# Kernel optimization log

Hardware: AMD Instinct MI355X
Metric: run time of the kernel (lower is better)

Reference implementation:

```python
import jax, jax.numpy as jnp
import numpy as np

N = 50000          # nodes
E = 1600000        # edges (avg degree 32)
F_IN = 128         # input feature dim
H = 8              # attention heads
D = 8              # per-head dim (concat -> H*D = 64)
NEG_SLOPE = 0.2    # PyG GATConv leaky relu slope


def setup_inputs() -> dict:
    key = jax.random.key(0)
    ks = jax.random.split(key, 16)
    x = jax.random.normal(ks[0], (N, F_IN), jnp.float32)
    edge_index = jax.random.randint(ks[1], (2, E), 0, N, jnp.int32)
    inp = {"x": x, "edge_index": edge_index}
    fin = F_IN
    for i in range(4):
        inp[f"W{i}"] = jax.random.normal(ks[2 + 3 * i], (fin, H * D), jnp.float32) * (1.0 / np.sqrt(fin))
        inp[f"att{i}"] = jax.random.normal(ks[3 + 3 * i], (2, H, D), jnp.float32) * 0.1
        inp[f"b{i}"] = jnp.zeros((H * D,), jnp.float32)
        fin = H * D
    return inp


def gat_layer(x, W, att, b, src, dst):
    # linear projection -> per-head features [N, H, D]
    h = (x @ W).reshape(-1, H, D)
    # per-node attention logits for src/dst roles [N, H]
    e_src = jnp.einsum("nhd,hd->nh", h, att[0])
    e_dst = jnp.einsum("nhd,hd->nh", h, att[1])
    # per-edge score [E, H]
    e = jax.nn.leaky_relu(e_src[src] + e_dst[dst], NEG_SLOPE)
    # segment softmax over incoming edges of each dst node
    m = jax.ops.segment_max(e, dst, num_segments=N)
    w = jnp.exp(e - m[dst])
    s = jax.ops.segment_sum(w, dst, num_segments=N)
    alpha = w / (s[dst] + 1e-16)
    # weighted message scatter-add: [E,H,D] -> [N,H,D]
    msg = alpha[:, :, None] * h[src]
    out = jax.ops.segment_sum(msg, dst, num_segments=N)
    return out.reshape(-1, H * D) + b


def reference(x, edge_index, W0, att0, b0, W1, att1, b1, W2, att2, b2, W3, att3, b3):
    src, dst = edge_index[0], edge_index[1]
    h = x
    params = [(W0, att0, b0), (W1, att1, b1), (W2, att2, b2), (W3, att3, b3)]
    for i, (W, att, b) in enumerate(params):
        h = gat_layer(h, W, att, b, src, dst)
        if i < len(params) - 1:
            h = jax.nn.elu(h)  # inter-layer activation as in PyG GAT (default ELU)
    return h
```

## Files before the change

### kernel.cpp

```cpp
#include <hip/hip_runtime.h>

#define N_NODES 50000
#define N_EDGES 1600000
#define HD 64
#define NH 8
#define NBKT 196
#define EPB 8192
#define GB1 196
#define SCAN_M (NBKT * GB1)
#define NB2 151
#define DCAP 8960
#define SEGB 2048
#define GBN 196

__device__ inline int wave_incl_scan(int v, int lane) {
#pragma unroll
    for (int o = 1; o < 64; o <<= 1) {
        int t = __shfl_up(v, o);
        if (lane >= o) v += t;
    }
    return v;
}

template <int F>
__device__ __forceinline__ void gemm_body16(
    int bx, int by, int t,
    const float* __restrict__ x, const float* __restrict__ W,
    const float* __restrict__ att,
    _Float16* __restrict__ h, float* __restrict__ es, float* __restrict__ ed) {
    int n = bx * 256 + t;
    int f0 = by * 16;
    int nc = (n < N_NODES) ? n : (N_NODES - 1);
    const float4* xrow = (const float4*)x + (size_t)nc * (F / 4);
    float acc[16];
#pragma unroll
    for (int i = 0; i < 16; i++) acc[i] = 0.f;
#pragma unroll 4
    for (int kk = 0; kk < F / 4; kk++) {
        float4 xv = xrow[kk];
        const float* Wk = W + (kk * 4) * 64 + f0;
#pragma unroll
        for (int i = 0; i < 16; i++)
            acc[i] += xv.x * Wk[i] + xv.y * Wk[64 + i] +
                      xv.z * Wk[128 + i] + xv.w * Wk[192 + i];
    }
    if (n >= N_NODES) return;

    float s0 = 0.f, s1 = 0.f, d0 = 0.f, d1 = 0.f;
#pragma unroll
    for (int i = 0; i < 8; i++) {
        s0 += acc[i] * att[f0 + i];
        d0 += acc[i] * att[64 + f0 + i];
    }
#pragma unroll
    for (int i = 8; i < 16; i++) {
        s1 += acc[i] * att[f0 + i];
        d1 += acc[i] * att[64 + f0 + i];
    }
    int hh = f0 >> 3;
    es[n * NH + hh] = s0; es[n * NH + hh + 1] = s1;
    ed[n * NH + hh] = d0; ed[n * NH + hh + 1] = d1;

    union { _Float16 hf[16]; uint4 u[2]; } cv;
#pragma unroll
    for (int i = 0; i < 16; i++) cv.hf[i] = (_Float16)acc[i];
    uint4* hp = (uint4*)(h + (size_t)n * HD + f0);
    hp[0] = cv.u[0];
    hp[1] = cv.u[1];
}

template <int F>
__global__ __launch_bounds__(256) void gemm_att_kernel(
    const float* __restrict__ x, const float* __restrict__ W,
    const float* __restrict__ att,
    _Float16* __restrict__ h, float* __restrict__ es, float* __restrict__ ed) {
    gemm_body16<F>(blockIdx.x, blockIdx.y, threadIdx.x, x, W, att, h, es, ed);
}

__global__ __launch_bounds__(256) void histA_gemm_kernel(
    const int* __restrict__ dst, int* __restrict__ offs,
    const float* __restrict__ x, const float* __restrict__ W,
    const float* __restrict__ att,
    _Float16* __restrict__ h, float* __restrict__ es, float* __restrict__ ed) {
    if (blockIdx.y < 4) {
        gemm_body16<128>(blockIdx.x, blockIdx.y, threadIdx.x, x, W, att, h, es, ed);
        return;
    }
    int bb = blockIdx.x;
    __shared__ int hist[NBKT];
    int t = threadIdx.x;
    if (t < NBKT) hist[t] = 0;
    __syncthreads();
    int base = bb * EPB;
#pragma unroll
    for (int k = 0; k < EPB / 256; k++) {
        int e = base + k * 256 + t;
        if (e < N_EDGES) atomicAdd(&hist[dst[e] >> 8], 1);
    }
    __syncthreads();
    if (t < NBKT) offs[t * GB1 + bb] = hist[t];
}

__global__ __launch_bounds__(256) void scanB1_kernel(int* __restrict__ offs,
                                                     int* __restrict__ part2) {
    __shared__ int wsum[4];
    int t = threadIdx.x, lane = t & 63, wv = t >> 6;
    int i = blockIdx.x * 256 + t;
    int v = (i < SCAN_M) ? offs[i] : 0;
    int inc = wave_incl_scan(v, lane);
    if (lane == 63) wsum[wv] = inc;
    __syncthreads();
    if (t == 0) {
        int a = 0;
        for (int k = 0; k < 4; k++) { int x = wsum[k]; wsum[k] = a; a += x; }
    }
    __syncthreads();
    int excl = wsum[wv] + inc - v;
    if (i < SCAN_M) offs[i] = excl;
    if (t == 255) part2[blockIdx.x] = wsum[wv] + inc;
}

__global__ __launch_bounds__(256) void scatC_kernel(const int* __restrict__ src,
                                                    const int* __restrict__ dst,
                                                    const int* __restrict__ offs,
                                                    const int* __restrict__ part2,
                                                    unsigned* __restrict__ ebuf) {
    __shared__ int cur[NBKT];
    __shared__ int base_s[NBKT];
    __shared__ int p2s[256];
    __shared__ int p2w[4];
    int t = threadIdx.x, lane = t & 63, wv = t >> 6;
    int v = (t < NB2) ? part2[t] : 0;
    int inc = wave_incl_scan(v, lane);
    if (lane == 63) p2w[wv] = inc;
    __syncthreads();
    if (t == 0) {
        int a = 0;
        for (int k = 0; k < 4; k++) { int x = p2w[k]; p2w[k] = a; a += x; }
    }
    __syncthreads();
    p2s[t] = p2w[wv] + inc - v;
    if (t < NBKT) cur[t] = 0;
    __syncthreads();
    if (t < NBKT) {
        int f = t * GB1 + blockIdx.x;
        base_s[t] = offs[f] + p2s[f >> 8];
    }
    __syncthreads();
    int base = blockIdx.x * EPB;
#pragma unroll
    for (int k = 0; k < EPB / 256; k++) {
        int e = base + k * 256 + t;
        if (e < N_EDGES) {
            int d = dst[e];
            int b = d >> 8;
            int r = atomicAdd(&cur[b], 1);
            ebuf[base_s[b] + r] = (unsigned)src[e] | ((unsigned)(d & 255) << 16);
        }
    }
}

__global__ __launch_bounds__(512) void csrD_kernel(const int* __restrict__ offs,
                                                   const int* __restrict__ part2,
                                                   const unsigned* __restrict__ ebuf,
                                                   int* __restrict__ rowptr,
                                                   unsigned short* __restrict__ csr) {
    __shared__ unsigned eb[DCAP];
    __shared__ int hist[SEGB];
    __shared__ int wsum[8];
    __shared__ int p2s[512];
    int b = blockIdx.x, t = threadIdx.x;
    int lane = t & 63, wv = t >> 6;
    {
        int v = (t < NB2) ? part2[t] : 0;
        int inc = wave_incl_scan(v, lane);
        if (lane == 63) wsum[wv] = inc;
        __syncthreads();
        if (t == 0) {
            int a = 0;
            for (int k = 0; k < 8; k++) { int x = wsum[k]; wsum[k] = a; a += x; }
        }
        __syncthreads();
        p2s[t] = wsum[wv] + inc - v;
        __syncthreads();
    }
    int f0 = b * GB1;
    int base = offs[f0] + p2s[f0 >> 8];
    int nxt;
    if (b == NBKT - 1) nxt = N_EDGES;
    else { int f1 = (b + 1) * GB1; nxt = offs[f1] + p2s[f1 >> 8]; }
    int nb = nxt - base;
    if (nb > DCAP) nb = DCAP;
    for (int i = t; i < SEGB; i += 512) hist[i] = 0;
    __syncthreads();
    for (int i = t; i < nb; i += 512) {
        unsigned v = ebuf[base + i];
        eb[i] = v;
        int bin = (int)((v >> 16) << 3) | (int)((v & 0xFFFFu) >> 13);
        atomicAdd(&hist[bin], 1);
    }
    __syncthreads();
    int b0 = t << 2;
    int loc0 = hist[b0], loc1 = hist[b0 + 1], loc2 = hist[b0 + 2], loc3 = hist[b0 + 3];
    int s = loc0 + loc1 + loc2 + loc3;
    int inc = wave_incl_scan(s, lane);
    if (lane == 63) wsum[wv] = inc;
    __syncthreads();
    if (t == 0) {
        int a = 0;
        for (int k = 0; k < 8; k++) { int x = wsum[k]; wsum[k] = a; a += x; }
    }
    __syncthreads();
    int run = wsum[wv] + inc - s;
    hist[b0] = run; run += loc0;
    hist[b0 + 1] = run; run += loc1;
    hist[b0 + 2] = run; run += loc2;
    hist[b0 + 3] = run;
    __syncthreads();
    if (t < 256) {
        int node = b * 256 + t;
        if (node < N_NODES) rowptr[node] = base + hist[t << 3];
    }
    if (b == 0 && t == 0) rowptr[N_NODES] = N_EDGES;
    __syncthreads();
    for (int i = t; i < nb; i += 512) {
        unsigned v = eb[i];
        int bin = (int)((v >> 16) << 3) | (int)((v & 0xFFFFu) >> 13);
        int r = atomicAdd(&hist[bin], 1);
        csr[base + r] = (unsigned short)(v & 0xFFFFu);
    }
}

__global__ __launch_bounds__(256) void agg_kernel(
    const uint4* __restrict__ h8, const float* __restrict__ es,
    const float* __restrict__ ed, const int* __restrict__ rowptr,
    const unsigned short* __restrict__ csr, const float4* __restrict__ b4,
    float4* __restrict__ out4, int apply_elu) {
    int t = threadIdx.x;
    int wv = t >> 6, L = t & 63;
    int n = blockIdx.x * 8 + wv * 2 + (L >> 5);
    int g = (L >> 3) & 3, o = L & 7;
    int beg = rowptr[n], end = rowptr[n + 1];
    float edn = ed[n * NH + o];
    int last = (end > beg) ? (end - 1) : 0;
    float acc[8] = {0.f, 0.f, 0.f, 0.f, 0.f, 0.f, 0.f, 0.f};
    float ssum = 0.f;
    int j = beg;
    for (; j + 16 <= end; j += 16) {
        int s0 = csr[j + g];
        int s1 = csr[j + 4 + g];
        int s2 = csr[j + 8 + g];
        int s3 = csr[j + 12 + g];
        uint4 hv0 = h8[s0 * 8 + o];
        uint4 hv1 = h8[s1 * 8 + o];
        uint4 hv2 = h8[s2 * 8 + o];
        uint4 hv3 = h8[s3 * 8 + o];
        float ev0 = es[s0 * NH + o];
        float ev1 = es[s1 * NH + o];
        float ev2 = es[s2 * NH + o];
        float ev3 = es[s3 * NH + o];
        float e0 = ev0 + edn; e0 = (e0 > 0.f) ? e0 : 0.2f * e0;
        float e1 = ev1 + edn; e1 = (e1 > 0.f) ? e1 : 0.2f * e1;
        float e2 = ev2 + edn; e2 = (e2 > 0.f) ? e2 : 0.2f * e2;
        float e3 = ev3 + edn; e3 = (e3 > 0.f) ? e3 : 0.2f * e3;
        float w0 = __expf(e0), w1 = __expf(e1);
        float w2 = __expf(e2), w3 = __expf(e3);
        union { uint4 u; _Float16 f[8]; } c0, c1, c2, c3;
        c0.u = hv0; c1.u = hv1; c2.u = hv2; c3.u = hv3;
#pragma unroll
        for (int i = 0; i < 8; i++) {
            acc[i] += w0 * (float)c0.f[i] + w1 * (float)c1.f[i];
            acc[i] += w2 * (float)c2.f[i] + w3 * (float)c3.f[i];
        }
        ssum += w0 + w1;
        ssum += w2 + w3;
    }
    if (j < end) {
        int i0 = j + g, i1 = j + 4 + g, i2 = j + 8 + g, i3 = j + 12 + g;
        int s0 = csr[(i0 < end) ? i0 : last];
        int s1 = csr[(i1 < end) ? i1 : last];
        int s2 = csr[(i2 < end) ? i2 : last];
        int s3 = csr[(i3 < end) ? i3 : last];
        uint4 hv0 = h8[s0 * 8 + o];
        uint4 hv1 = h8[s1 * 8 + o];
        uint4 hv2 = h8[s2 * 8 + o];
        uint4 hv3 = h8[s3 * 8 + o];
        float ev0 = es[s0 * NH + o];
        float ev1 = es[s1 * NH + o];
        float ev2 = es[s2 * NH + o];
        float ev3 = es[s3 * NH + o];
        float e0 = ev0 + edn; e0 = (e0 > 0.f) ? e0 : 0.2f * e0;
        float e1 = ev1 + edn; e1 = (e1 > 0.f) ? e1 : 0.2f * e1;
        float e2 = ev2 + edn; e2 = (e2 > 0.f) ? e2 : 0.2f * e2;
        float e3 = ev3 + edn; e3 = (e3 > 0.f) ? e3 : 0.2f * e3;
        float w0 = (i0 < end) ? __expf(e0) : 0.f;
        float w1 = (i1 < end) ? __expf(e1) : 0.f;
        float w2 = (i2 < end) ? __expf(e2) : 0.f;
        float w3 = (i3 < end) ? __expf(e3) : 0.f;
        union { uint4 u; _Float16 f[8]; } c0, c1, c2, c3;
        c0.u = hv0; c1.u = hv1; c2.u = hv2; c3.u = hv3;
#pragma unroll
        for (int i = 0; i < 8; i++) {
            acc[i] += w0 * (float)c0.f[i] + w1 * (float)c1.f[i];
            acc[i] += w2 * (float)c2.f[i] + w3 * (float)c3.f[i];
        }
        ssum += w0 + w1;
        ssum += w2 + w3;
    }
#pragma unroll
    for (int i = 0; i < 8; i++) {
        acc[i] += __shfl_xor(acc[i], 8);
        acc[i] += __shfl_xor(acc[i], 16);
    }
    ssum += __shfl_xor(ssum, 8);
    ssum += __shfl_xor(ssum, 16);

    if (g == 0) {
        float inv = 1.f / (ssum + 1e-16f);
        float4 bv0 = b4[2 * o], bv1 = b4[2 * o + 1];
        float4 r0, r1;
        r0.x = acc[0] * inv + bv0.x; r0.y = acc[1] * inv + bv0.y;
        r0.z = acc[2] * inv + bv0.z; r0.w = acc[3] * inv + bv0.w;
        r1.x = acc[4] * inv + bv1.x; r1.y = acc[5] * inv + bv1.y;
        r1.z = acc[6] * inv + bv1.z; r1.w = acc[7] * inv + bv1.w;
        if (apply_elu) {
            r0.x = (r0.x > 0.f) ? r0.x : (__expf(r0.x) - 1.f);
            r0.y = (r0.y > 0.f) ? r0.y : (__expf(r0.y) - 1.f);
            r0.z = (r0.z > 0.f) ? r0.z : (__expf(r0.z) - 1.f);
            r0.w = (r0.w > 0.f) ? r0.w : (__expf(r0.w) - 1.f);
            r1.x = (r1.x > 0.f) ? r1.x : (__expf(r1.x) - 1.f);
            r1.y = (r1.y > 0.f) ? r1.y : (__expf(r1.y) - 1.f);
            r1.z = (r1.z > 0.f) ? r1.z : (__expf(r1.z) - 1.f);
            r1.w = (r1.w > 0.f) ? r1.w : (__expf(r1.w) - 1.f);
        }
        out4[n * 16 + 2 * o] = r0;
        out4[n * 16 + 2 * o + 1] = r1;
    }
}

extern "C" void kernel_launch(void* const* d_in, const int* in_sizes, int n_in,
                              void* d_out, int out_size, void* d_ws, size_t ws_size,
                              hipStream_t stream) {
    const float* x   = (const float*)d_in[0];
    const int*   ei  = (const int*)d_in[1];
    const int*   src = ei;
    const int*   dst = ei + N_EDGES;
    const float* W[4]   = {(const float*)d_in[2], (const float*)d_in[5],
                           (const float*)d_in[8], (const float*)d_in[11]};
    const float* att[4] = {(const float*)d_in[3], (const float*)d_in[6],
                           (const float*)d_in[9], (const float*)d_in[12]};
    const float* bb[4]  = {(const float*)d_in[4], (const float*)d_in[7],
                           (const float*)d_in[10], (const float*)d_in[13]};

    char* wsb = (char*)d_ws;
    size_t off = 0;
    auto alloc = [&](size_t bytes) -> void* {
        size_t a = (off + 255) & ~(size_t)255;
        off = a + bytes;
        return (void*)(wsb + a);
    };
    int*            offs   = (int*)alloc((size_t)SCAN_M * 4);
    int*            part2  = (int*)alloc((size_t)NB2 * 4);
    unsigned*       ebuf   = (unsigned*)alloc((size_t)N_EDGES * 4);
    int*            rowptr = (int*)alloc((size_t)(N_NODES + 1) * 4);
    unsigned short* csr    = (unsigned short*)alloc((size_t)N_EDGES * 2);
    _Float16*       h      = (_Float16*)alloc((size_t)N_NODES * HD * 2);
    float*          es     = (float*)alloc((size_t)N_NODES * NH * 4);
    float*          ed     = (float*)alloc((size_t)N_NODES * NH * 4);
    float*          act0   = (float*)alloc((size_t)N_NODES * HD * 4);
    float*          act1   = (float*)alloc((size_t)N_NODES * HD * 4);

    const int GA = N_NODES / 8;
    const dim3 GG(GBN, 4);
    const dim3 GF(GBN, 5);

    histA_gemm_kernel<<<GF, 256, 0, stream>>>(dst, offs, x, W[0], att[0],
                                              h, es, ed);
    scanB1_kernel<<<NB2, 256, 0, stream>>>(offs, part2);
    scatC_kernel<<<GB1, 256, 0, stream>>>(src, dst, offs, part2, ebuf);
    csrD_kernel<<<NBKT, 512, 0, stream>>>(offs, part2, ebuf, rowptr, csr);

    agg_kernel<<<GA, 256, 0, stream>>>((const uint4*)h, es, ed, rowptr, csr,
                                       (const float4*)bb[0], (float4*)act0, 1);
    gemm_att_kernel<64><<<GG, 256, 0, stream>>>(act0, W[1], att[1], h, es, ed);
    agg_kernel<<<GA, 256, 0, stream>>>((const uint4*)h, es, ed, rowptr, csr,
                                       (const float4*)bb[1], (float4*)act1, 1);
    gemm_att_kernel<64><<<GG, 256, 0, stream>>>(act1, W[2], att[2], h, es, ed);
    agg_kernel<<<GA, 256, 0, stream>>>((const uint4*)h, es, ed, rowptr, csr,
                                       (const float4*)bb[2], (float4*)act0, 1);
    gemm_att_kernel<64><<<GG, 256, 0, stream>>>(act0, W[3], att[3], h, es, ed);
    agg_kernel<<<GA, 256, 0, stream>>>((const uint4*)h, es, ed, rowptr, csr,
                                       (const float4*)bb[3], (float4*)d_out, 0);
}
```

Measured before the change: 335.1 us.

## Fuse aggregation with next layer's projection and attention logits

Merges each inter-layer aggregation kernel with the following 64x64 projection and attention-logit kernel. Each block loads the next layer's weights into shared memory, aggregates 8 nodes and applies ELU into shared memory, then computes the projected fp16 features and per-head es/ed directly. This removes three kernel launches and the fp32 activation write and re-read between layers. In exchange it double-buffers h/es/ed and adds a per-block weight load into roughly 17 KB of shared memory, which may lower occupancy for the latency-bound gather.

```diff
diff --git a/kernel.cpp b/kernel.cpp
--- a/kernel.cpp
+++ b/kernel.cpp
@@ -67,14 +67,6 @@
     uint4* hp = (uint4*)(h + (size_t)n * HD + f0);
     hp[0] = cv.u[0];
     hp[1] = cv.u[1];
-}
-
-template <int F>
-__global__ __launch_bounds__(256) void gemm_att_kernel(
-    const float* __restrict__ x, const float* __restrict__ W,
-    const float* __restrict__ att,
-    _Float16* __restrict__ h, float* __restrict__ es, float* __restrict__ ed) {
-    gemm_body16<F>(blockIdx.x, blockIdx.y, threadIdx.x, x, W, att, h, es, ed);
 }
 
 __global__ __launch_bounds__(256) void histA_gemm_kernel(
@@ -231,89 +223,92 @@
     }
 }
 
+#define AGG_LOOP()                                                          \
+    int beg = rowptr[n], end = rowptr[n + 1];                               \
+    float edn = ed_in[n * NH + o];                                          \
+    int last = (end > beg) ? (end - 1) : 0;                                 \
+    float acc[8] = {0.f, 0.f, 0.f, 0.f, 0.f, 0.f, 0.f, 0.f};                \
+    float ssum = 0.f;                                                       \
+    int j = beg;                                                            \
+    for (; j + 16 <= end; j += 16) {                                        \
+        int s0 = csr[j + g];                                                \
+        int s1 = csr[j + 4 + g];                                            \
+        int s2 = csr[j + 8 + g];                                            \
+        int s3 = csr[j + 12 + g];                                           \
+        uint4 hv0 = h8[s0 * 8 + o];                                         \
+        uint4 hv1 = h8[s1 * 8 + o];                                         \
+        uint4 hv2 = h8[s2 * 8 + o];                                         \
+        uint4 hv3 = h8[s3 * 8 + o];                                         \
+        float ev0 = es_in[s0 * NH + o];                                     \
+        float ev1 = es_in[s1 * NH + o];                                     \
+        float ev2 = es_in[s2 * NH + o];                                     \
+        float ev3 = es_in[s3 * NH + o];                                     \
+        float e0 = ev0 + edn; e0 = (e0 > 0.f) ? e0 : 0.2f * e0;             \
+        float e1 = ev1 + edn; e1 = (e1 > 0.f) ? e1 : 0.2f * e1;             \
+        float e2 = ev2 + edn; e2 = (e2 > 0.f) ? e2 : 0.2f * e2;             \
+        float e3 = ev3 + edn; e3 = (e3 > 0.f) ? e3 : 0.2f * e3;             \
+        float w0 = __expf(e0), w1 = __expf(e1);                             \
+        float w2 = __expf(e2), w3 = __expf(e3);                             \
+        union { uint4 u; _Float16 f[8]; } c0, c1, c2, c3;                   \
+        c0.u = hv0; c1.u = hv1; c2.u = hv2; c3.u = hv3;                     \
+        _Pragma("unroll")                                                   \
+        for (int i = 0; i < 8; i++) {                                       \
+            acc[i] += w0 * (float)c0.f[i] + w1 * (float)c1.f[i];            \
+            acc[i] += w2 * (float)c2.f[i] + w3 * (float)c3.f[i];            \
+        }                                                                   \
+        ssum += w0 + w1;                                                    \
+        ssum += w2 + w3;                                                    \
+    }                                                                       \
+    if (j < end) {                                                          \
+        int i0 = j + g, i1 = j + 4 + g, i2 = j + 8 + g, i3 = j + 12 + g;    \
+        int s0 = csr[(i0 < end) ? i0 : last];                               \
+        int s1 = csr[(i1 < end) ? i1 : last];                               \
+        int s2 = csr[(i2 < end) ? i2 : last];                               \
+        int s3 = csr[(i3 < end) ? i3 : last];                               \
+        uint4 hv0 = h8[s0 * 8 + o];                                         \
+        uint4 hv1 = h8[s1 * 8 + o];                                         \
+        uint4 hv2 = h8[s2 * 8 + o];                                         \
+        uint4 hv3 = h8[s3 * 8 + o];                                         \
+        float ev0 = es_in[s0 * NH + o];                                     \
+        float ev1 = es_in[s1 * NH + o];                                     \
+        float ev2 = es_in[s2 * NH + o];                                     \
+        float ev3 = es_in[s3 * NH + o];                                     \
+        float e0 = ev0 + edn; e0 = (e0 > 0.f) ? e0 : 0.2f * e0;             \
+        float e1 = ev1 + edn; e1 = (e1 > 0.f) ? e1 : 0.2f * e1;             \
+        float e2 = ev2 + edn; e2 = (e2 > 0.f) ? e2 : 0.2f * e2;             \
+        float e3 = ev3 + edn; e3 = (e3 > 0.f) ? e3 : 0.2f * e3;             \
+        float w0 = (i0 < end) ? __expf(e0) : 0.f;                           \
+        float w1 = (i1 < end) ? __expf(e1) : 0.f;                           \
+        float w2 = (i2 < end) ? __expf(e2) : 0.f;                           \
+        float w3 = (i3 < end) ? __expf(e3) : 0.f;                           \
+        union { uint4 u; _Float16 f[8]; } c0, c1, c2, c3;                   \
+        c0.u = hv0; c1.u = hv1; c2.u = hv2; c3.u = hv3;                     \
+        _Pragma("unroll")                                                   \
+        for (int i = 0; i < 8; i++) {                                       \
+            acc[i] += w0 * (float)c0.f[i] + w1 * (float)c1.f[i];            \
+            acc[i] += w2 * (float)c2.f[i] + w3 * (float)c3.f[i];            \
+        }                                                                   \
+        ssum += w0 + w1;                                                    \
+        ssum += w2 + w3;                                                    \
+    }                                                                       \
+    _Pragma("unroll")                                                       \
+    for (int i = 0; i < 8; i++) {                                           \
+        acc[i] += __shfl_xor(acc[i], 8);                                    \
+        acc[i] += __shfl_xor(acc[i], 16);                                   \
+    }                                                                       \
+    ssum += __shfl_xor(ssum, 8);                                            \
+    ssum += __shfl_xor(ssum, 16);
+
 __global__ __launch_bounds__(256) void agg_kernel(
-    const uint4* __restrict__ h8, const float* __restrict__ es,
-    const float* __restrict__ ed, const int* __restrict__ rowptr,
+    const uint4* __restrict__ h8, const float* __restrict__ es_in,
+    const float* __restrict__ ed_in, const int* __restrict__ rowptr,
     const unsigned short* __restrict__ csr, const float4* __restrict__ b4,
     float4* __restrict__ out4, int apply_elu) {
     int t = threadIdx.x;
     int wv = t >> 6, L = t & 63;
     int n = blockIdx.x * 8 + wv * 2 + (L >> 5);
     int g = (L >> 3) & 3, o = L & 7;
-    int beg = rowptr[n], end = rowptr[n + 1];
-    float edn = ed[n * NH + o];
-    int last = (end > beg) ? (end - 1) : 0;
-    float acc[8] = {0.f, 0.f, 0.f, 0.f, 0.f, 0.f, 0.f, 0.f};
-    float ssum = 0.f;
-    int j = beg;
-    for (; j + 16 <= end; j += 16) {
-        int s0 = csr[j + g];
-        int s1 = csr[j + 4 + g];
-        int s2 = csr[j + 8 + g];
-        int s3 = csr[j + 12 + g];
-        uint4 hv0 = h8[s0 * 8 + o];
-        uint4 hv1 = h8[s1 * 8 + o];
-        uint4 hv2 = h8[s2 * 8 + o];
-        uint4 hv3 = h8[s3 * 8 + o];
-        float ev0 = es[s0 * NH + o];
-        float ev1 = es[s1 * NH + o];
-        float ev2 = es[s2 * NH + o];
-        float ev3 = es[s3 * NH + o];
-        float e0 = ev0 + edn; e0 = (e0 > 0.f) ? e0 : 0.2f * e0;
-        float e1 = ev1 + edn; e1 = (e1 > 0.f) ? e1 : 0.2f * e1;
-        float e2 = ev2 + edn; e2 = (e2 > 0.f) ? e2 : 0.2f * e2;
-        float e3 = ev3 + edn; e3 = (e3 > 0.f) ? e3 : 0.2f * e3;
-        float w0 = __expf(e0), w1 = __expf(e1);
-        float w2 = __expf(e2), w3 = __expf(e3);
-        union { uint4 u; _Float16 f[8]; } c0, c1, c2, c3;
-        c0.u = hv0; c1.u = hv1; c2.u = hv2; c3.u = hv3;
-#pragma unroll
-        for (int i = 0; i < 8; i++) {
-            acc[i] += w0 * (float)c0.f[i] + w1 * (float)c1.f[i];
-            acc[i] += w2 * (float)c2.f[i] + w3 * (float)c3.f[i];
-        }
-        ssum += w0 + w1;
-        ssum += w2 + w3;
-    }
-    if (j < end) {
-        int i0 = j + g, i1 = j + 4 + g, i2 = j + 8 + g, i3 = j + 12 + g;
-        int s0 = csr[(i0 < end) ? i0 : last];
-        int s1 = csr[(i1 < end) ? i1 : last];
-        int s2 = csr[(i2 < end) ? i2 : last];
-        int s3 = csr[(i3 < end) ? i3 : last];
-        uint4 hv0 = h8[s0 * 8 + o];
-        uint4 hv1 = h8[s1 * 8 + o];
-        uint4 hv2 = h8[s2 * 8 + o];
-        uint4 hv3 = h8[s3 * 8 + o];
-        float ev0 = es[s0 * NH + o];
-        float ev1 = es[s1 * NH + o];
-        float ev2 = es[s2 * NH + o];
-        float ev3 = es[s3 * NH + o];
-        float e0 = ev0 + edn; e0 = (e0 > 0.f) ? e0 : 0.2f * e0;
-        float e1 = ev1 + edn; e1 = (e1 > 0.f) ? e1 : 0.2f * e1;
-        float e2 = ev2 + edn; e2 = (e2 > 0.f) ? e2 : 0.2f * e2;
-        float e3 = ev3 + edn; e3 = (e3 > 0.f) ? e3 : 0.2f * e3;
-        float w0 = (i0 < end) ? __expf(e0) : 0.f;
-        float w1 = (i1 < end) ? __expf(e1) : 0.f;
-        float w2 = (i2 < end) ? __expf(e2) : 0.f;
-        float w3 = (i3 < end) ? __expf(e3) : 0.f;
-        union { uint4 u; _Float16 f[8]; } c0, c1, c2, c3;
-        c0.u = hv0; c1.u = hv1; c2.u = hv2; c3.u = hv3;
-#pragma unroll
-        for (int i = 0; i < 8; i++) {
-            acc[i] += w0 * (float)c0.f[i] + w1 * (float)c1.f[i];
-            acc[i] += w2 * (float)c2.f[i] + w3 * (float)c3.f[i];
-        }
-        ssum += w0 + w1;
-        ssum += w2 + w3;
-    }
-#pragma unroll
-    for (int i = 0; i < 8; i++) {
-        acc[i] += __shfl_xor(acc[i], 8);
-        acc[i] += __shfl_xor(acc[i], 16);
-    }
-    ssum += __shfl_xor(ssum, 8);
-    ssum += __shfl_xor(ssum, 16);
+    AGG_LOOP()
 
     if (g == 0) {
         float inv = 1.f / (ssum + 1e-16f);
@@ -338,6 +333,85 @@
     }
 }
 
+__global__ __launch_bounds__(256) void aggemm_kernel(
+    const uint4* __restrict__ h8, const float* __restrict__ es_in,
+    const float* __restrict__ ed_in, const int* __restrict__ rowptr,
+    const unsigned short* __restrict__ csr, const float4* __restrict__ b4,
+    const float* __restrict__ Wn, const float* __restrict__ attn,
+    _Float16* __restrict__ h_out, float* __restrict__ es_out,
+    float* __restrict__ ed_out) {
+    __shared__ alignas(16) float wTp[32 * 132];
+    __shared__ alignas(16) float outs[8][64];
+    int t = threadIdx.x;
+    {
+        const float4* W4 = (const float4*)Wn;
+#pragma unroll
+        for (int q = 0; q < 4; q++) {
+            int idx4 = q * 256 + t;
+            float4 wv4 = W4[idx4];
+            int base = idx4 << 2;
+            int k = base >> 6, fb = base & 63;
+            float2* p0 = (float2*)&wTp[(fb >> 1) * 132 + k * 2];
+            float2* p1 = (float2*)&wTp[((fb >> 1) + 1) * 132 + k * 2];
+            p0->x = wv4.x; p0->y = wv4.y;
+            p1->x = wv4.z; p1->y = wv4.w;
+        }
+    }
+    int wv = t >> 6, L = t & 63;
+    int slot = wv * 2 + (L >> 5);
+    int n = blockIdx.x * 8 + slot;
+    int g = (L >> 3) & 3, o = L & 7;
+    AGG_LOOP()
+
+    if (g == 0) {
+        float inv = 1.f / (ssum + 1e-16f);
+        float4 bv0 = b4[2 * o], bv1 = b4[2 * o + 1];
+        float4 r0, r1;
+        r0.x = acc[0] * inv + bv0.x; r0.y = acc[1] * inv + bv0.y;
+        r0.z = acc[2] * inv + bv0.z; r0.w = acc[3] * inv + bv0.w;
+        r1.x = acc[4] * inv + bv1.x; r1.y = acc[5] * inv + bv1.y;
+        r1.z = acc[6] * inv + bv1.z; r1.w = acc[7] * inv + bv1.w;
+        r0.x = (r0.x > 0.f) ? r0.x : (__expf(r0.x) - 1.f);
+        r0.y = (r0.y > 0.f) ? r0.y : (__expf(r0.y) - 1.f);
+        r0.z = (r0.z > 0.f) ? r0.z : (__expf(r0.z) - 1.f);
+        r0.w = (r0.w > 0.f) ? r0.w : (__expf(r0.w) - 1.f);
+        r1.x = (r1.x > 0.f) ? r1.x : (__expf(r1.x) - 1.f);
+        r1.y = (r1.y > 0.f) ? r1.y : (__expf(r1.y) - 1.f);
+        r1.z = (r1.z > 0.f) ? r1.z : (__expf(r1.z) - 1.f);
+        r1.w = (r1.w > 0.f) ? r1.w : (__expf(r1.w) - 1.f);
+        float4* os = (float4*)&outs[slot][0];
+        os[2 * o] = r0;
+        os[2 * o + 1] = r1;
+    }
+    __syncthreads();
+
+    int li = L & 31;
+    int f0 = li << 1;
+    const float* wrow = &wTp[li * 132];
+    float h0 = 0.f, h1 = 0.f;
+#pragma unroll
+    for (int k4 = 0; k4 < 64; k4 += 4) {
+        float4 ov = *(const float4*)&outs[slot][k4];
+        float4 wa = *(const float4*)&wrow[k4 * 2];
+        float4 wb = *(const float4*)&wrow[k4 * 2 + 4];
+        h0 += ov.x * wa.x + ov.y * wa.z + ov.z * wb.x + ov.w * wb.z;
+        h1 += ov.x * wa.y + ov.y * wa.w + ov.z * wb.y + ov.w * wb.w;
+    }
+    float sa = h0 * attn[f0] + h1 * attn[f0 + 1];
+    float da = h0 * attn[64 + f0] + h1 * attn[64 + f0 + 1];
+    sa += __shfl_xor(sa, 1); sa += __shfl_xor(sa, 2);
+    da += __shfl_xor(da, 1); da += __shfl_xor(da, 2);
+    if ((li & 3) == 0) {
+        int hh = li >> 2;
+        es_out[n * NH + hh] = sa;
+        ed_out[n * NH + hh] = da;
+    }
+    union { _Float16 hf[2]; unsigned u; } cv;
+    cv.hf[0] = (_Float16)h0;
+    cv.hf[1] = (_Float16)h1;
+    *(unsigned*)(h_out + (size_t)n * HD + f0) = cv.u;
+}
+
 extern "C" void kernel_launch(void* const* d_in, const int* in_sizes, int n_in,
                               void* d_out, int out_size, void* d_ws, size_t ws_size,
                               hipStream_t stream) {
@@ -364,31 +438,32 @@
     unsigned*       ebuf   = (unsigned*)alloc((size_t)N_EDGES * 4);
     int*            rowptr = (int*)alloc((size_t)(N_NODES + 1) * 4);
     unsigned short* csr    = (unsigned short*)alloc((size_t)N_EDGES * 2);
-    _Float16*       h      = (_Float16*)alloc((size_t)N_NODES * HD * 2);
-    float*          es     = (float*)alloc((size_t)N_NODES * NH * 4);
-    float*          ed     = (float*)alloc((size_t)N_NODES * NH * 4);
-    float*          act0   = (float*)alloc((size_t)N_NODES * HD * 4);
-    float*          act1   = (float*)alloc((size_t)N_NODES * HD * 4);
+    _Float16*       h_a    = (_Float16*)alloc((size_t)N_NODES * HD * 2);
+    float*          es_a   = (float*)alloc((size_t)N_NODES * NH * 4);
+    float*          ed_a   = (float*)alloc((size_t)N_NODES * NH * 4);
+    _Float16*       h_b    = (_Float16*)alloc((size_t)N_NODES * HD * 2);
+    float*          es_b   = (float*)alloc((size_t)N_NODES * NH * 4);
+    float*          ed_b   = (float*)alloc((size_t)N_NODES * NH * 4);
 
     const int GA = N_NODES / 8;
-    const dim3 GG(GBN, 4);
     const dim3 GF(GBN, 5);
 
     histA_gemm_kernel<<<GF, 256, 0, stream>>>(dst, offs, x, W[0], att[0],
-                                              h, es, ed);
+                                              h_a, es_a, ed_a);
     scanB1_kernel<<<NB2, 256, 0, stream>>>(offs, part2);
     scatC_kernel<<<GB1, 256, 0, stream>>>(src, dst, offs, part2, ebuf);
     csrD_kernel<<<NBKT, 512, 0, stream>>>(offs, part2, ebuf, rowptr, csr);
 
-    agg_kernel<<<GA, 256, 0, stream>>>((const uint4*)h, es, ed, rowptr, csr,
-                                       (const float4*)bb[0], (float4*)act0, 1);
-    gemm_att_kernel<64><<<GG, 256, 0, stream>>>(act0, W[1], att[1], h, es, ed);
-    agg_kernel<<<GA, 256, 0, stream>>>((const uint4*)h, es, ed, rowptr, csr,
-                                       (const float4*)bb[1], (float4*)act1, 1);
-    gemm_att_kernel<64><<<GG, 256, 0, stream>>>(act1, W[2], att[2], h, es, ed);
-    agg_kernel<<<GA, 256, 0, stream>>>((const uint4*)h, es, ed, rowptr, csr,
-                                       (const float4*)bb[2], (float4*)act0, 1);
-    gemm_att_kernel<64><<<GG, 256, 0, stream>>>(act0, W[3], att[3], h, es, ed);
-    agg_kernel<<<GA, 256, 0, stream>>>((const uint4*)h, es, ed, rowptr, csr,
-                                       (const float4*)bb[3], (float4*)d_out, 0);
-}
+    aggemm_kernel<<<GA, 256, 0, stream>>>((const uint4*)h_a, es_a, ed_a,
+                                          rowptr, csr, (const float4*)bb[0],
+                                          W[1], att[1], h_b, es_b, ed_b);
+    aggemm_kernel<<<GA, 256, 0, stream>>>((const uint4*)h_b, es_b, ed_b,
+                                          rowptr, csr, (const float4*)bb[1],
+                                          W[2], att[2], h_a, es_a, ed_a);
+    aggemm_kernel<<<GA, 256, 0, stream>>>((const uint4*)h_a, es_a, ed_a,
+                                          rowptr, csr, (const float4*)bb[2],
+                                          W[3], att[3], h_b, es_b, ed_b);
+    agg_kernel<<<GA, 256, 0, stream>>>((const uint4*)h_b, es_b, ed_b,
+                                       rowptr, csr, (const float4*)bb[3],
+                                       (float4*)d_out, 0);
+}
```

Measured after the change: 304.2 us. 1.1x faster.
